# Performance work log

Hardware: AMD Instinct MI355X
Metric: run time of the kernel (lower is better)

## Reference

```python
import jax, jax.numpy as jnp
import numpy as np

K = 81  # num_classes + 1 background
CH = [512, 1024, 512, 256, 256, 256]          # per-level feature channels
MBOX = [4, 6, 6, 6, 4, 4]                     # default boxes per location
# extra layers: (out_ch, in_ch, kernel, stride, pad), per _make_extra_layers for SSD300
EXTRA = [(256, 1024, 1, 1, 0), (512, 256, 3, 2, 1),
         (128, 512, 1, 1, 0), (256, 128, 3, 2, 1),
         (128, 256, 1, 1, 0), (256, 128, 3, 1, 0),
         (128, 256, 1, 1, 0), (256, 128, 3, 1, 0)]


def _conv(x, w, b, s, p):
    y = jax.lax.conv_general_dilated(x, w, (s, s), [(p, p), (p, p)],
                                     dimension_numbers=('NCHW', 'OIHW', 'NCHW'))
    return y + b[None, :, None, None]


def setup_inputs() -> dict:
    key = jax.random.key(0)
    ks = iter(jax.random.split(key, 64))
    d = {}
    d['feat0'] = jax.random.normal(next(ks), (16, 512, 38, 38), jnp.float32)
    d['feat1'] = jax.random.normal(next(ks), (16, 1024, 19, 19), jnp.float32)
    d['l2norm_w'] = jnp.full((512,), 20.0, jnp.float32)  # init constant = l2norm_scale
    for i, (o, ci, k, s, p) in enumerate(EXTRA):
        d[f'e{i}_w'] = jax.random.normal(next(ks), (o, ci, k, k), jnp.float32) / np.sqrt(ci * k * k)
        d[f'e{i}_b'] = jnp.zeros((o,), jnp.float32)
    for i, (c, m) in enumerate(zip(CH, MBOX)):
        sc = 1.0 / np.sqrt(c * 9)
        d[f'cls{i}_w'] = jax.random.normal(next(ks), (m * K, c, 3, 3), jnp.float32) * sc
        d[f'cls{i}_b'] = jnp.zeros((m * K,), jnp.float32)
        d[f'box{i}_w'] = jax.random.normal(next(ks), (m * 4, c, 3, 3), jnp.float32) * sc
        d[f'box{i}_b'] = jnp.zeros((m * 4,), jnp.float32)
    return d


def _forward(feat0, feat1, l2norm_w, extra_params, head_params):
    # L2Norm on conv4_3
    norm = jnp.sqrt(jnp.sum(feat0 * feat0, axis=1, keepdims=True)) + 1e-10
    f0 = l2norm_w[None, :, None, None] * feat0 / norm
    features = [f0, feat1]
    x = feat1
    for idx, ((w, b), (_, _, k, s, p)) in enumerate(zip(extra_params, EXTRA)):
        x = jax.nn.relu(_conv(x, w, b, s, p))
        if idx % 2 == 1:
            features.append(x)
    confs, locs = [], []
    for f, (cw, cb, bw, bb) in zip(features, head_params):
        n = f.shape[0]
        # (N, m*K, H, W) -> (N, H, W, m*K) -> (N, H*W*m, K)
        confs.append(_conv(f, cw, cb, 1, 1).transpose(0, 2, 3, 1).reshape(n, -1, K))
        locs.append(_conv(f, bw, bb, 1, 1).transpose(0, 2, 3, 1).reshape(n, -1, 4))
    conf = jnp.concatenate(confs, axis=1)  # (N, 8732, 81)
    loc = jnp.concatenate(locs, axis=1)    # (N, 8732, 4)
    return jnp.concatenate([conf, loc], axis=-1)  # packed (N, 8732, 85)


def reference(feat0, feat1, l2norm_w,
              e0_w, e0_b, e1_w, e1_b, e2_w, e2_b, e3_w, e3_b,
              e4_w, e4_b, e5_w, e5_b, e6_w, e6_b, e7_w, e7_b,
              cls0_w, cls0_b, box0_w, box0_b,
              cls1_w, cls1_b, box1_w, box1_b,
              cls2_w, cls2_b, box2_w, box2_b,
              cls3_w, cls3_b, box3_w, box3_b,
              cls4_w, cls4_b, box4_w, box4_b,
              cls5_w, cls5_b, box5_w, box5_b):
    extra_params = [(e0_w, e0_b), (e1_w, e1_b), (e2_w, e2_b), (e3_w, e3_b),
                    (e4_w, e4_b), (e5_w, e5_b), (e6_w, e6_b), (e7_w, e7_b)]
    head_params = [(cls0_w, cls0_b, box0_w, box0_b), (cls1_w, cls1_b, box1_w, box1_b),
                   (cls2_w, cls2_b, box2_w, box2_b), (cls3_w, cls3_b, box3_w, box3_b),
                   (cls4_w, cls4_b, box4_w, box4_b), (cls5_w, cls5_b, box5_w, box5_b)]
    return _forward(feat0, feat1, l2norm_w, extra_params, head_params)
```

## Files before the change

kernel.cpp:

```cpp
#include <hip/hip_runtime.h>
#include <hip/hip_bf16.h>

typedef __attribute__((ext_vector_type(8))) short short8;
typedef __attribute__((ext_vector_type(4))) float f32x4;

__device__ __forceinline__ short f2bf(float f) {
  unsigned u = __float_as_uint(f);
  u += 0x7fffu + ((u >> 16) & 1u);
  return (short)(u >> 16);
}

__device__ __forceinline__ void gload16(const short* g, short* l) {
  __builtin_amdgcn_global_load_lds(
      (const __attribute__((address_space(1))) unsigned int*)g,
      (__attribute__((address_space(3))) unsigned int*)l, 16, 0, 0);
}

struct WSeg { const float* src; short* dst; int Ci; int S; int elems; };
struct WPrep { WSeg seg[20]; };

struct PrepPack {
  const float* f0; short* f0dst; const float* l2w;
  const float* f1; short* f1dst;
  WPrep wp; int wtotal;
  int nF0, nF1;
};

__global__ __launch_bounds__(256) void prep_kernel(PrepPack pp) {
  __shared__ float red[8][32];
  __shared__ float sscale[32];
  __shared__ float tile[32][33];
  int id = blockIdx.x;
  if (id < pp.nF0) {
    constexpr int C = 512, H = 38, W = 38, Wp = 40, nstride = 1600, hh = 1;
    int bx = id % 46, n = id / 46;
    int P = H * W;
    int p0 = bx * 32;
    int pl = threadIdx.x & 31, cg = threadIdx.x >> 5;
    const float* s = pp.f0 + (size_t)n * C * P;
    float ss = 0.f;
    int p = p0 + pl;
    if (p < P) {
      for (int k = 0; k < 64; ++k) {
        float v = s[(size_t)(cg * 64 + k) * P + p];
        ss += v * v;
      }
    }
    red[cg][pl] = ss;
    __syncthreads();
    if (threadIdx.x < 32) {
      float tot = 0.f;
      #pragma unroll
      for (int g = 0; g < 8; ++g) tot += red[g][threadIdx.x];
      sscale[threadIdx.x] = 1.0f / (sqrtf(tot) + 1e-10f);
    }
    __syncthreads();
    for (int ct = 0; ct < 16; ++ct) {
      int c0 = ct * 32;
      __syncthreads();
      #pragma unroll
      for (int i = 0; i < 4; ++i) {
        int cl = cg + i * 8;
        tile[cl][pl] = (p < P) ? s[(size_t)(c0 + cl) * P + p] : 0.f;
      }
      __syncthreads();
      #pragma unroll
      for (int i = 0; i < 4; ++i) {
        int pll = cg + i * 8;
        int pp2 = p0 + pll;
        if (pp2 >= P) continue;
        int c = c0 + pl;
        float v = tile[pl][pll] * pp.l2w[c] * sscale[pll];
        int y = pp2 / W, x = pp2 - y * W;
        pp.f0dst[((size_t)n * nstride + (y + hh) * Wp + (x + hh)) * C + c] = f2bf(v);
      }
    }
    return;
  }
  id -= pp.nF0;
  if (id < pp.nF1) {
    constexpr int C = 1024, H = 19, W = 19, Wp = 21, nstride = 441, hh = 1;
    int bx = id % 12, byc = (id / 12) % 32, n = id / (12 * 32);
    int P = H * W;
    int p0 = bx * 32, c0 = byc * 32;
    int tp = threadIdx.x & 31, tr = threadIdx.x >> 5;
    const float* s = pp.f1 + (size_t)n * C * P;
    #pragma unroll
    for (int i = 0; i < 4; ++i) {
      int cl = tr + i * 8;
      int p = p0 + tp;
      tile[cl][tp] = (p < P) ? s[(size_t)(c0 + cl) * P + p] : 0.f;
    }
    __syncthreads();
    #pragma unroll
    for (int i = 0; i < 4; ++i) {
      int pl = tr + i * 8;
      int p = p0 + pl;
      if (p >= P) continue;
      int c = c0 + tp;
      float v = tile[tp][pl];
      int y = p / W, x = p - y * W;
      pp.f1dst[((size_t)n * nstride + (y + hh) * Wp + (x + hh)) * C + c] = f2bf(v);
    }
    return;
  }
  id -= pp.nF1;
  int i = id * 256 + threadIdx.x;
  if (i >= pp.wtotal) return;
  int local = i;
  int si = 0;
  while (local >= pp.wp.seg[si].elems) { local -= pp.wp.seg[si].elems; ++si; }
  WSeg sg = pp.wp.seg[si];
  int ci = local % sg.Ci;
  int q  = local / sg.Ci;
  int s  = q % sg.S;
  int co = q / sg.S;
  float v = sg.src[((size_t)co * sg.Ci + ci) * sg.S + s];
  sg.dst[local] = f2bf(v);
}

struct ConvP {
  const short* in;
  const short* w;
  const float* b1;
  const float* b2;
  short* out_bf;
  float* out_f;
  int M, Ci, iHp, iWp, Ho, Wo, Co;
  int S, kdim, stride, ioff;
  int oWp, onstride, oh;
  int mbox, row_base;
};

template<int BM, int BN, int BK, int WM, int WN, bool HEAD>
__device__ __forceinline__ void conv_core(const ConvP p, int bx, int by) {
  constexpr int NT  = WM * WN * 64;
  constexpr int CPR = BK / 8;
  constexpr int RPP = NT / CPR;
  constexpr int NRA = BM / RPP, NRB = BN / RPP;
  constexpr int AM = BM / WM / 16, AN = BN / WN / 16, KK = BK / 32;
  constexpr int ABUF = BM * BK, BBUF = BN * BK;
  __shared__ short As[2 * ABUF];
  __shared__ short Bs[2 * BBUF];
  const int t = threadIdx.x, lane = t & 63, wave = t >> 6;
  const int HW = p.Ho * p.Wo;
  const int sr = t / CPR;
  const int slot = ((t & (CPR - 1)) ^ (sr & (CPR - 1))) * 8;

  const short* aBase[NRA];
  const short* bBase[NRB];
  #pragma unroll
  for (int i = 0; i < NRA; ++i) {
    int pos = bx * BM + sr + i * RPP; if (pos >= p.M) pos = p.M - 1;
    int n = pos / HW, rem = pos - n * HW;
    int yo = rem / p.Wo, xo = rem - yo * p.Wo;
    aBase[i] = p.in + ((size_t)(n * p.iHp + yo * p.stride + p.ioff) * p.iWp
                      + xo * p.stride + p.ioff) * p.Ci + slot;
  }
  #pragma unroll
  for (int i = 0; i < NRB; ++i) {
    int co = by * BN + sr + i * RPP; if (co >= p.Co) co = p.Co - 1;
    bBase[i] = p.w + (size_t)co * p.S * p.Ci + slot;
  }
  const int cs = p.Ci / BK;
  const int total = p.S * cs;

  auto stage = [&](int buf, int aoff, int boff) {
    #pragma unroll
    for (int i = 0; i < NRA; ++i)
      gload16(aBase[i] + aoff, &As[buf * ABUF + i * (NT * 8) + t * 8]);
    #pragma unroll
    for (int i = 0; i < NRB; ++i)
      gload16(bBase[i] + boff, &Bs[buf * BBUF + i * (NT * 8) + t * 8]);
  };

  int ntap = 0, ncc = 0;
  auto aoff_cur = [&]() -> int {
    if (p.S == 1) return ncc * BK;
    unsigned dy = (unsigned)ntap / 3u;
    int dx = ntap - (int)dy * 3;
    return ((int)dy * p.iWp + dx) * p.Ci + ncc * BK;
  };

  stage(0, aoff_cur(), 0);
  ++ncc; if (ncc == cs) { ncc = 0; ++ntap; }
  __syncthreads();

  f32x4 acc[AM][AN];
  #pragma unroll
  for (int i = 0; i < AM; ++i)
    #pragma unroll
    for (int j = 0; j < AN; ++j)
      acc[i][j] = (f32x4){0.f, 0.f, 0.f, 0.f};

  const int wr = (wave / WN) * (BM / WM), wc = (wave % WN) * (BN / WN);
  const int lrow = lane & 15, kgrp = lane >> 4;

  int cur = 0;
  for (int ks = 0; ks < total; ++ks) {
    if (ks + 1 < total) {
      stage(cur ^ 1, aoff_cur(), (ks + 1) * BK);
      ++ncc; if (ncc == cs) { ncc = 0; ++ntap; }
    }
    const short* aRd0 = &As[cur * ABUF];
    const short* bRd0 = &Bs[cur * BBUF];
    short8 a[AM][KK], b[AN][KK];
    #pragma unroll
    for (int i = 0; i < AM; ++i) {
      int r = wr + i * 16 + lrow;
      #pragma unroll
      for (int kk = 0; kk < KK; ++kk) {
        int ch = ((kk << 2) | kgrp) ^ (r & (CPR - 1));
        a[i][kk] = *reinterpret_cast<const short8*>(aRd0 + r * BK + ch * 8);
      }
    }
    #pragma unroll
    for (int j = 0; j < AN; ++j) {
      int r = wc + j * 16 + lrow;
      #pragma unroll
      for (int kk = 0; kk < KK; ++kk) {
        int ch = ((kk << 2) | kgrp) ^ (r & (CPR - 1));
        b[j][kk] = *reinterpret_cast<const short8*>(bRd0 + r * BK + ch * 8);
      }
    }
    #pragma unroll
    for (int kk = 0; kk < KK; ++kk)
      #pragma unroll
      for (int i = 0; i < AM; ++i)
        #pragma unroll
        for (int j = 0; j < AN; ++j)
          acc[i][j] = __builtin_amdgcn_mfma_f32_16x16x32_bf16(a[i][kk], b[j][kk], acc[i][j], 0, 0, 0);
    __syncthreads();
    cur ^= 1;
  }

  const int mk = p.mbox * 81;
  const int rb_ = (lane >> 4) * 4, cl_ = lane & 15;
  #pragma unroll
  for (int i = 0; i < AM; ++i)
    #pragma unroll
    for (int j = 0; j < AN; ++j)
      #pragma unroll
      for (int q = 0; q < 4; ++q) {
        int po = bx * BM + wr + i * 16 + rb_ + q;
        int co = by * BN + wc + j * 16 + cl_;
        if (po >= p.M || co >= p.Co) continue;
        float v = acc[i][j][q];
        if (!HEAD) {
          int n2 = po / HW, sp = po - n2 * HW;
          int y = sp / p.Wo, x = sp - y * p.Wo;
          float v2 = fmaxf(v + p.b1[co], 0.f);
          p.out_bf[((size_t)n2 * p.onstride + (y + p.oh) * p.oWp + (x + p.oh)) * p.Co + co] = f2bf(v2);
        } else {
          int n2 = po / HW, sp = po - n2 * HW;
          int mi, col; float bias;
          if (co < mk) { mi = co / 81; col = co - mi * 81; bias = p.b1[co]; }
          else { int cbx = co - mk; mi = cbx >> 2; col = 81 + (cbx & 3); bias = p.b2[cbx]; }
          size_t orow = (size_t)n2 * 8732 + p.row_base + (size_t)sp * p.mbox + mi;
          p.out_f[orow * 85 + col] = v + bias;
        }
      }
}

__global__ __launch_bounds__(256) void conv_tile64(ConvP p) {
  conv_core<64, 64, 128, 2, 2, false>(p, blockIdx.x, blockIdx.y);
}

struct HeadPack { ConvP L[6]; int g0[6]; int nbyA[6]; int sb[56]; };

__global__ __launch_bounds__(512) void head_grouped(HeadPack h) {
  int p = blockIdx.x, x = p & 7, s = p >> 3;
  if (s >= h.sb[48 + x]) return;
  int li = 0;
  #pragma unroll
  for (int i = 1; i < 6; ++i) if (s >= h.sb[i * 8 + x]) li = i;
  int r = s - h.sb[li * 8 + x];
  int nby = h.nbyA[li];
  int k = r / nby, by = r - k * nby;
  int bx = ((x - h.g0[li]) & 7) + 8 * k;
  conv_core<128, 128, 64, 2, 4, true>(h.L[li], bx, by);
}

extern "C" void kernel_launch(void* const* d_in, const int* in_sizes, int n_in,
                              void* d_out, int out_size, void* d_ws, size_t ws_size,
                              hipStream_t stream) {
  const float* feat0 = (const float*)d_in[0];
  const float* feat1 = (const float*)d_in[1];
  const float* l2w   = (const float*)d_in[2];
  const float* ew[8]; const float* eb[8];
  for (int i = 0; i < 8; ++i) { ew[i] = (const float*)d_in[3 + 2 * i]; eb[i] = (const float*)d_in[4 + 2 * i]; }
  const float* cw[6]; const float* cb[6]; const float* bw[6]; const float* bb[6];
  for (int i = 0; i < 6; ++i) {
    cw[i] = (const float*)d_in[19 + 4 * i]; cb[i] = (const float*)d_in[20 + 4 * i];
    bw[i] = (const float*)d_in[21 + 4 * i]; bb[i] = (const float*)d_in[22 + 4 * i];
  }
  float* out = (float*)d_out;
  char* ws = (char*)d_ws;
  size_t off = 0;
  auto alloc = [&](size_t bytes) -> char* {
    char* p = ws + off;
    off = (off + bytes + 255) & ~(size_t)255;
    return p;
  };
  char* featStart = ws + off;
  short* f0b = (short*)alloc((size_t)16 * 40 * 40 * 512 * 2);
  short* f1b = (short*)alloc((size_t)16 * 21 * 21 * 1024 * 2);
  short* xe0 = (short*)alloc((size_t)16 * 21 * 21 * 256 * 2);
  short* f2b = (short*)alloc((size_t)16 * 12 * 12 * 512 * 2);
  short* xe2 = (short*)alloc((size_t)16 * 12 * 12 * 128 * 2);
  short* f3b = (short*)alloc((size_t)16 * 7 * 7 * 256 * 2);
  short* xe4 = (short*)alloc((size_t)16 * 5 * 5 * 128 * 2);
  short* f4b = (short*)alloc((size_t)16 * 5 * 5 * 256 * 2);
  short* xe6 = (short*)alloc((size_t)16 * 3 * 3 * 128 * 2);
  short* f5b = (short*)alloc((size_t)16 * 3 * 3 * 256 * 2);
  size_t featBytes = (size_t)((ws + off) - featStart);

  static const int eCo[8] = {256, 512, 128, 256, 128, 256, 128, 256};
  static const int eCi[8] = {1024, 256, 512, 128, 256, 128, 256, 128};
  static const int eS[8]  = {1, 9, 1, 9, 1, 9, 1, 9};
  static const int mbox[6] = {4, 6, 6, 6, 4, 4};
  static const int hCi[6] = {512, 1024, 512, 256, 256, 256};

  WPrep wp; int total = 0; int segi = 0;
  short* ewb[8]; short* hwb[6];
  for (int i = 0; i < 8; ++i) {
    int e = eCo[i] * eCi[i] * eS[i];
    ewb[i] = (short*)alloc((size_t)e * 2);
    wp.seg[segi++] = {ew[i], ewb[i], eCi[i], eS[i], e};
    total += e;
  }
  for (int L = 0; L < 6; ++L) {
    int co = mbox[L] * 85;
    int e = co * hCi[L] * 9;
    hwb[L] = (short*)alloc((size_t)e * 2);
    int ecls = mbox[L] * 81 * hCi[L] * 9;
    wp.seg[segi++] = {cw[L], hwb[L], hCi[L], 9, ecls};
    wp.seg[segi++] = {bw[L], hwb[L] + (size_t)mbox[L] * 81 * 9 * hCi[L], hCi[L], 9, e - ecls};
    total += e;
  }

  hipMemsetAsync(featStart, 0, featBytes, stream);

  PrepPack pp;
  pp.f0 = feat0; pp.f0dst = f0b; pp.l2w = l2w;
  pp.f1 = feat1; pp.f1dst = f1b;
  pp.wp = wp; pp.wtotal = total;
  pp.nF0 = 46 * 16;
  pp.nF1 = 12 * 32 * 16;
  int nPrep = pp.nF0 + pp.nF1 + (total + 255) / 256;
  prep_kernel<<<dim3(nPrep), 256, 0, stream>>>(pp);

  auto mkP = [&](const short* in, const short* wbuf, const float* b1, const float* b2,
                 short* outb, float* outf, int Ci, int iHp, int iWp, int Ho, int Wo,
                 int Co, int S, int kd, int st, int ioff, int oWp, int onstride, int oh,
                 int m, int rb) {
    ConvP p{}; p.in = in; p.w = wbuf; p.b1 = b1; p.b2 = b2; p.out_bf = outb; p.out_f = outf;
    p.M = 16 * Ho * Wo; p.Ci = Ci; p.iHp = iHp; p.iWp = iWp; p.Ho = Ho; p.Wo = Wo; p.Co = Co;
    p.S = S; p.kdim = kd; p.stride = st; p.ioff = ioff;
    p.oWp = oWp; p.onstride = onstride; p.oh = oh; p.mbox = m; p.row_base = rb;
    return p;
  };
  auto run64 = [&](ConvP p) {
    conv_tile64<<<dim3((p.M + 63) / 64, (p.Co + 63) / 64), 256, 0, stream>>>(p);
  };

  run64(mkP(f1b, ewb[0], eb[0], nullptr, xe0, nullptr, 1024, 21, 21, 19, 19, 256, 1, 1, 1, 1, 21, 441, 1, 0, 0));
  run64(mkP(xe0, ewb[1], eb[1], nullptr, f2b, nullptr,  256, 21, 21, 10, 10, 512, 9, 3, 2, 0, 12, 144, 1, 0, 0));
  run64(mkP(f2b, ewb[2], eb[2], nullptr, xe2, nullptr,  512, 12, 12, 10, 10, 128, 1, 1, 1, 1, 12, 144, 1, 0, 0));
  run64(mkP(xe2, ewb[3], eb[3], nullptr, f3b, nullptr,  128, 12, 12,  5,  5, 256, 9, 3, 2, 0,  7,  49, 1, 0, 0));
  run64(mkP(f3b, ewb[4], eb[4], nullptr, xe4, nullptr,  256,  7,  7,  5,  5, 128, 1, 1, 1, 1,  5,  25, 0, 0, 0));
  run64(mkP(xe4, ewb[5], eb[5], nullptr, f4b, nullptr,  128,  5,  5,  3,  3, 256, 9, 3, 1, 0,  5,  25, 1, 0, 0));
  run64(mkP(f4b, ewb[6], eb[6], nullptr, xe6, nullptr,  256,  5,  5,  3,  3, 128, 1, 1, 1, 1,  3,   9, 0, 0, 0));
  run64(mkP(xe6, ewb[7], eb[7], nullptr, f5b, nullptr,  128,  3,  3,  1,  1, 256, 9, 3, 1, 0,  3,   9, 1, 0, 0));

  HeadPack h;
  h.L[0] = mkP(f1b, hwb[1], cb[1], bb[1], nullptr, out, 1024, 21, 21, 19, 19, 6 * 85, 9, 3, 1, 0, 0, 0, 0, 6, 5776);
  h.L[1] = mkP(f0b, hwb[0], cb[0], bb[0], nullptr, out,  512, 40, 40, 38, 38, 4 * 85, 9, 3, 1, 0, 0, 0, 0, 4, 0);
  h.L[2] = mkP(f2b, hwb[2], cb[2], bb[2], nullptr, out,  512, 12, 12, 10, 10, 6 * 85, 9, 3, 1, 0, 0, 0, 0, 6, 7942);
  h.L[3] = mkP(f3b, hwb[3], cb[3], bb[3], nullptr, out,  256,  7,  7,  5,  5, 6 * 85, 9, 3, 1, 0, 0, 0, 0, 6, 8542);
  h.L[4] = mkP(f4b, hwb[4], cb[4], bb[4], nullptr, out,  256,  5,  5,  3,  3, 4 * 85, 9, 3, 1, 0, 0, 0, 0, 4, 8692);
  h.L[5] = mkP(f5b, hwb[5], cb[5], bb[5], nullptr, out,  256,  3,  3,  1,  1, 4 * 85, 9, 3, 1, 0, 0, 0, 0, 4, 8728);

  int gid = 0;
  for (int x = 0; x < 8; ++x) h.sb[x] = 0;
  for (int li = 0; li < 6; ++li) {
    int nbx = (h.L[li].M + 127) / 128;
    h.nbyA[li] = (h.L[li].Co + 127) / 128;
    h.g0[li] = gid & 7;
    for (int x = 0; x < 8; ++x) {
      int f = ((x - gid) % 8 + 8) % 8;
      int cnt = (f < nbx) ? (nbx - f + 7) / 8 : 0;
      h.sb[(li + 1) * 8 + x] = h.sb[li * 8 + x] + h.nbyA[li] * cnt;
    }
    gid += nbx;
  }
  int maxSlots = 0;
  for (int x = 0; x < 8; ++x) if (h.sb[48 + x] > maxSlots) maxSlots = h.sb[48 + x];
  head_grouped<<<dim3(8 * maxSlots), 512, 0, stream>>>(h);
}
```

Before: 355.7 us.

## Fuse six small extra-layer convs into one per-image LDS-resident tail kernel

Replaces the six separate tiled conv launches for extra layers 2-7 with a single kernel that launches one 512-thread block per image. Intermediate activations stay in swizzled LDS buffers, and only the feature maps the heads need are written to global memory. The goal is to remove five launch overheads and the global round trips for the tiny intermediate tensors. The cost is that only 16 blocks run, so most of the GPU sits idle during the tail, and the weights are read from global memory without any tiling.

Result: slower. 436.1 us (+22.6%).

```diff
diff --git a/kernel.cpp b/kernel.cpp
--- a/kernel.cpp
+++ b/kernel.cpp
@@ -266,6 +266,99 @@
   conv_core<64, 64, 128, 2, 2, false>(p, blockIdx.x, blockIdx.y);
 }
 
+template<int iHp, int iWp, int Ci, int ioff, int stride, int kdim, int S,
+         int Ho, int Wo, int Co, int oWp, int oh, bool GIN, bool GOUT>
+__device__ __forceinline__ void tail_layer(const short* __restrict__ gin,
+    const short* lin, const short* __restrict__ w, const float* __restrict__ bias,
+    short* lout, short* gout) {
+  constexpr int M = Ho * Wo;
+  constexpr int FM = (M + 15) / 16;
+  constexpr int FC = Co / 16;
+  const int lane = threadIdx.x & 63, wave = threadIdx.x >> 6;
+  const int l15 = lane & 15, kg = lane >> 4;
+  for (int f = wave; f < FM * FC; f += 8) {
+    int fm = f % FM, fc = f / FM;
+    f32x4 acc = (f32x4){0.f, 0.f, 0.f, 0.f};
+    int r = fm * 16 + l15; if (r >= M) r = M - 1;
+    int yo = r / Wo, xo = r - yo * Wo;
+    int co = fc * 16 + l15;
+    const short* wrow = w + (size_t)co * S * Ci;
+    #pragma unroll
+    for (int s = 0; s < S; ++s) {
+      int dy = s / kdim, dx = s - dy * kdim;
+      int ipos = (yo * stride + dy + ioff) * iWp + (xo * stride + dx + ioff);
+      #pragma unroll
+      for (int ck = 0; ck < Ci / 32; ++ck) {
+        int ci0 = ck * 32 + kg * 8;
+        short8 a;
+        if (GIN) {
+          a = *reinterpret_cast<const short8*>(gin + (size_t)ipos * Ci + ci0);
+        } else {
+          int sw = (ci0 >> 3) ^ (ipos & 7);
+          a = *reinterpret_cast<const short8*>(lin + ipos * Ci + sw * 8);
+        }
+        short8 b = *reinterpret_cast<const short8*>(wrow + s * Ci + ci0);
+        acc = __builtin_amdgcn_mfma_f32_16x16x32_bf16(a, b, acc, 0, 0, 0);
+      }
+    }
+    #pragma unroll
+    for (int q = 0; q < 4; ++q) {
+      int pos = fm * 16 + kg * 4 + q;
+      if (pos >= M) continue;
+      int y = pos / Wo, x = pos - y * Wo;
+      float v = fmaxf(acc[q] + bias[co], 0.f);
+      short bv = f2bf(v);
+      int opos = (y + oh) * oWp + (x + oh);
+      int swc = (co >> 3) ^ (opos & 7);
+      lout[opos * Co + swc * 8 + (co & 7)] = bv;
+      if (GOUT) gout[(size_t)opos * Co + co] = bv;
+    }
+  }
+}
+
+__device__ __forceinline__ void zero_lds(short* p, int nshorts) {
+  int* q = (int*)p;
+  for (int i = threadIdx.x; i < nshorts / 2; i += 512) q[i] = 0;
+}
+
+struct TailPack {
+  const short* f2b; short* f3b; short* f4b; short* f5b;
+  const short* w2; const short* w3; const short* w4; const short* w5;
+  const short* w6; const short* w7;
+  const float* b2; const float* b3; const float* b4; const float* b5;
+  const float* b6; const float* b7;
+};
+
+__global__ __launch_bounds__(512) void tail_kernel(TailPack tp) {
+  __shared__ short sm[30976];
+  short* R0 = sm;
+  short* R1 = sm + 18432;
+  int n = blockIdx.x;
+  zero_lds(R0, 18432); __syncthreads();
+  tail_layer<12, 12, 512, 1, 1, 1, 1, 10, 10, 128, 12, 1, true, false>(
+      tp.f2b + (size_t)n * 144 * 512, nullptr, tp.w2, tp.b2, R0, nullptr);
+  __syncthreads();
+  zero_lds(R1, 12544); __syncthreads();
+  tail_layer<12, 12, 128, 0, 2, 3, 9, 5, 5, 256, 7, 1, false, true>(
+      nullptr, R0, tp.w3, tp.b3, R1, tp.f3b + (size_t)n * 49 * 256);
+  __syncthreads();
+  zero_lds(R0, 3200); __syncthreads();
+  tail_layer<7, 7, 256, 1, 1, 1, 1, 5, 5, 128, 5, 0, false, false>(
+      nullptr, R1, tp.w4, tp.b4, R0, nullptr);
+  __syncthreads();
+  zero_lds(R1, 6400); __syncthreads();
+  tail_layer<5, 5, 128, 0, 1, 3, 9, 3, 3, 256, 5, 1, false, true>(
+      nullptr, R0, tp.w5, tp.b5, R1, tp.f4b + (size_t)n * 25 * 256);
+  __syncthreads();
+  zero_lds(R0, 1152); __syncthreads();
+  tail_layer<5, 5, 256, 1, 1, 1, 1, 3, 3, 128, 3, 0, false, false>(
+      nullptr, R1, tp.w6, tp.b6, R0, nullptr);
+  __syncthreads();
+  zero_lds(R1, 2304); __syncthreads();
+  tail_layer<3, 3, 128, 0, 1, 3, 9, 1, 1, 256, 3, 1, false, true>(
+      nullptr, R0, tp.w7, tp.b7, R1, tp.f5b + (size_t)n * 9 * 256);
+}
+
 struct HeadPack { ConvP L[6]; int g0[6]; int nbyA[6]; int sb[56]; };
 
 __global__ __launch_bounds__(512) void head_grouped(HeadPack h) {
@@ -307,11 +400,8 @@
   short* f1b = (short*)alloc((size_t)16 * 21 * 21 * 1024 * 2);
   short* xe0 = (short*)alloc((size_t)16 * 21 * 21 * 256 * 2);
   short* f2b = (short*)alloc((size_t)16 * 12 * 12 * 512 * 2);
-  short* xe2 = (short*)alloc((size_t)16 * 12 * 12 * 128 * 2);
   short* f3b = (short*)alloc((size_t)16 * 7 * 7 * 256 * 2);
-  short* xe4 = (short*)alloc((size_t)16 * 5 * 5 * 128 * 2);
   short* f4b = (short*)alloc((size_t)16 * 5 * 5 * 256 * 2);
-  short* xe6 = (short*)alloc((size_t)16 * 3 * 3 * 128 * 2);
   short* f5b = (short*)alloc((size_t)16 * 3 * 3 * 256 * 2);
   size_t featBytes = (size_t)((ws + off) - featStart);
 
@@ -366,12 +456,12 @@
 
   run64(mkP(f1b, ewb[0], eb[0], nullptr, xe0, nullptr, 1024, 21, 21, 19, 19, 256, 1, 1, 1, 1, 21, 441, 1, 0, 0));
   run64(mkP(xe0, ewb[1], eb[1], nullptr, f2b, nullptr,  256, 21, 21, 10, 10, 512, 9, 3, 2, 0, 12, 144, 1, 0, 0));
-  run64(mkP(f2b, ewb[2], eb[2], nullptr, xe2, nullptr,  512, 12, 12, 10, 10, 128, 1, 1, 1, 1, 12, 144, 1, 0, 0));
-  run64(mkP(xe2, ewb[3], eb[3], nullptr, f3b, nullptr,  128, 12, 12,  5,  5, 256, 9, 3, 2, 0,  7,  49, 1, 0, 0));
-  run64(mkP(f3b, ewb[4], eb[4], nullptr, xe4, nullptr,  256,  7,  7,  5,  5, 128, 1, 1, 1, 1,  5,  25, 0, 0, 0));
-  run64(mkP(xe4, ewb[5], eb[5], nullptr, f4b, nullptr,  128,  5,  5,  3,  3, 256, 9, 3, 1, 0,  5,  25, 1, 0, 0));
-  run64(mkP(f4b, ewb[6], eb[6], nullptr, xe6, nullptr,  256,  5,  5,  3,  3, 128, 1, 1, 1, 1,  3,   9, 0, 0, 0));
-  run64(mkP(xe6, ewb[7], eb[7], nullptr, f5b, nullptr,  128,  3,  3,  1,  1, 256, 9, 3, 1, 0,  3,   9, 1, 0, 0));
+
+  TailPack tp;
+  tp.f2b = f2b; tp.f3b = f3b; tp.f4b = f4b; tp.f5b = f5b;
+  tp.w2 = ewb[2]; tp.w3 = ewb[3]; tp.w4 = ewb[4]; tp.w5 = ewb[5]; tp.w6 = ewb[6]; tp.w7 = ewb[7];
+  tp.b2 = eb[2]; tp.b3 = eb[3]; tp.b4 = eb[4]; tp.b5 = eb[5]; tp.b6 = eb[6]; tp.b7 = eb[7];
+  tail_kernel<<<dim3(16), 512, 0, stream>>>(tp);
 
   HeadPack h;
   h.L[0] = mkP(f1b, hwb[1], cb[1], bb[1], nullptr, out, 1024, 21, 21, 19, 19, 6 * 85, 9, 3, 1, 0, 0, 0, 0, 6, 5776);
```
